# Optimization experiments

Measured on AMD Instinct MI355X. Metric: run time of the kernel, lower is better.

The kernel has to match this reference:

```python
import jax, jax.numpy as jnp
import numpy as np

N_NODES = 100000
H_DIM = 128
N_RELS = 90   # num_rels*2 inside RGCN
N_BASES = 4
N_EDGES = 800000


def setup_inputs() -> dict:
    key = jax.random.key(0)
    k_emb, k_w, k_comp, k_r, k_norm, k_src, k_dst, k_b = jax.random.split(key, 8)
    h = jnp.arange(N_NODES, dtype=jnp.int64 if jax.config.jax_enable_x64 else jnp.int32)
    r = jax.random.randint(k_r, (N_EDGES,), 0, N_RELS)
    norm = jax.random.uniform(k_norm, (N_EDGES, 1), dtype=jnp.float32)
    src = jax.random.randint(k_src, (N_EDGES,), 0, N_NODES)
    dst = jax.random.randint(k_dst, (N_EDGES,), 0, N_NODES)
    # learned params (embedding table stands in for the word2vec-initialized table)
    emb_table = jax.random.normal(k_emb, (N_NODES, H_DIM), dtype=jnp.float32) * 0.02
    weight = jax.random.normal(k_w, (N_BASES, H_DIM, H_DIM), dtype=jnp.float32) * (1.0 / np.sqrt(H_DIM))
    w_comp = jax.random.normal(k_comp, (N_RELS, N_BASES), dtype=jnp.float32) * 0.5
    h_bias = jnp.zeros((H_DIM,), dtype=jnp.float32)
    return {"h": h, "r": r, "norm": norm, "src": src, "dst": dst,
            "emb_table": emb_table, "weight": weight, "w_comp": w_comp, "h_bias": h_bias}


def reference(h, r, norm, src, dst, emb_table, weight, w_comp, h_bias):
    # Input layer: embedding lookup on node ids  -> [N, D]
    x = emb_table[h]
    # Basis decomposition: project node feats onto each basis once  -> [N, B, D]
    # (avoids materializing per-edge [D,D] relation matrices)
    xb = jnp.einsum('ni,bio->nbo', x, weight)
    # Per-edge message: combine basis projections with relation coefficients
    coeff = w_comp[r]                       # [E, B]
    msg = jnp.einsum('ebo,eb->eo', xb[src], coeff)   # [E, D]
    msg = msg * norm                        # edge norm [E,1]
    # scatter-mean over destination nodes
    agg = jax.ops.segment_sum(msg, dst, num_segments=N_NODES)          # [N, D]
    cnt = jax.ops.segment_sum(jnp.ones((msg.shape[0],), msg.dtype), dst,
                              num_segments=N_NODES)                    # [N]
    node_repr = agg / jnp.maximum(cnt, 1.0)[:, None]
    # bias (RelGraphConv default bias=True); activation=None, self_loop=False, dropout=0
    node_repr = node_repr + h_bias
    return node_repr
```

## Files before the change

kernel.cpp:

```cpp
#include <hip/hip_runtime.h>
#include <hip/hip_bf16.h>

#define N_NODES 100000
#define H_DIM   128
#define N_RELS  90
#define N_BASES 4
#define N_EDGES 800000
#define SCAN_NB 391
#define NBLK    6250

typedef __attribute__((ext_vector_type(8))) __bf16 bf16x8;
typedef __attribute__((ext_vector_type(4))) float  floatx4;

#define WT_OFF     0
#define CNTS_OFF   131072
#define OFFS_OFF   531072
#define CURS_OFF   931072
#define BSUM_OFF   1331072
#define BPRE_OFF   1332672
#define RECS_OFF   1334272

__device__ __forceinline__ float bs2f(unsigned short s) {
    union { unsigned u; float f; } x; x.u = ((unsigned)s) << 16; return x.f;
}
__device__ __forceinline__ unsigned short f2bs(float f) {
    unsigned u = __float_as_uint(f);
    return (unsigned short)((u + 0x7fffu + ((u >> 16) & 1u)) >> 16);
}
__device__ __forceinline__ float ldf(const void* p, size_t i, int isbf) {
    return isbf ? bs2f(((const unsigned short*)p)[i]) : ((const float*)p)[i];
}
__device__ __forceinline__ int detect_bf(const void* norm) {
    const unsigned* w = (const unsigned*)norm;
    int hits = 0;
#pragma unroll
    for (int i = 0; i < 16; ++i) {
        unsigned b1 = (w[i] >> 8) & 0xffu;
        hits += (b1 >= 0x30u && b1 <= 0x3fu) ? 1 : 0;
    }
    return hits >= 12;
}

__global__ __launch_bounds__(256) void prep_count_k(const void* __restrict__ weight,
                                                    unsigned short* __restrict__ wt,
                                                    const int* __restrict__ dst,
                                                    int* __restrict__ counts,
                                                    const void* __restrict__ norm) {
    int b = blockIdx.x;
    if (b < 256) {
        int isbf = detect_bf(norm);
        int tid = b * 256 + threadIdx.x;
        int o = tid >> 9, c = tid & 511;
        int bb = c >> 7, i = c & 127;
        wt[tid] = f2bs(ldf(weight, (size_t)bb * 16384 + (size_t)i * 128 + o, isbf));
    } else {
        int e = (b - 256) * 256 + threadIdx.x;
        if (e < N_EDGES) atomicAdd(&counts[dst[e]], 1);
    }
}

__global__ __launch_bounds__(256) void scanA(const int* __restrict__ counts,
                                             int* __restrict__ offs, int* __restrict__ bsum) {
    __shared__ int s[256];
    int t = threadIdx.x, i = blockIdx.x * 256 + t;
    int v = (i < N_NODES) ? counts[i] : 0;
    s[t] = v; __syncthreads();
    for (int off = 1; off < 256; off <<= 1) {
        int x = (t >= off) ? s[t - off] : 0;
        __syncthreads(); s[t] += x; __syncthreads();
    }
    if (i < N_NODES) offs[i] = s[t] - v;
    if (t == 255) bsum[blockIdx.x] = s[255];
}

__global__ __launch_bounds__(512) void scanB(const int* __restrict__ bsum, int* __restrict__ bpre) {
    __shared__ int s[512];
    int t = threadIdx.x;
    int v = (t < SCAN_NB) ? bsum[t] : 0;
    s[t] = v; __syncthreads();
    for (int off = 1; off < 512; off <<= 1) {
        int x = (t >= off) ? s[t - off] : 0;
        __syncthreads(); s[t] += x; __syncthreads();
    }
    if (t < SCAN_NB) bpre[t] = s[t] - v;
}

__global__ __launch_bounds__(256) void scanC(int* __restrict__ offs, const int* __restrict__ bpre,
                                             int* __restrict__ cursor) {
    int i = blockIdx.x * 256 + threadIdx.x;
    if (i < N_NODES) {
        int o = offs[i] + bpre[i >> 8];
        offs[i] = o; cursor[i] = o;
    }
}

__global__ __launch_bounds__(256) void fill_k(const int* __restrict__ r, const void* __restrict__ norm,
                                              const int* __restrict__ src, const int* __restrict__ dst,
                                              const int* __restrict__ h,
                                              int* __restrict__ cursor,
                                              unsigned long long* __restrict__ recs) {
    int e = blockIdx.x * 256 + threadIdx.x;
    if (e >= N_EDGES) return;
    int isbf = detect_bf(norm);
    float nm = ldf(norm, e, isbf);
    unsigned lo = (unsigned)h[src[e]] | ((unsigned)r[e] << 20);
    unsigned long long rc = (unsigned long long)lo
                          | ((unsigned long long)__float_as_uint(nm) << 32);
    int pos = atomicAdd(&cursor[dst[e]], 1);
    __builtin_nontemporal_store(rc, &recs[pos]);
}

__global__ __launch_bounds__(256) void fused_k(const int* __restrict__ counts,
                                               const int* __restrict__ offs,
                                               const unsigned long long* __restrict__ recs,
                                               const void* __restrict__ emb,
                                               const unsigned short* __restrict__ wt,
                                               const void* __restrict__ bias,
                                               const void* __restrict__ wcomp,
                                               const void* __restrict__ norm,
                                               void* __restrict__ out) {
    int isbf = detect_bf(norm);
    __shared__ float wc[N_RELS * 4];
    __shared__ __align__(16) unsigned short y[16][520];
    for (int t = threadIdx.x; t < N_RELS * 4; t += 256) wc[t] = ldf(wcomp, t, isbf);
    __syncthreads();

    int t = threadIdx.x;
    int lane = t & 63;
    int w = t >> 6;
    int g = lane >> 4, j = lane & 15;
    int blk = blockIdx.x;
    int dloc = w * 4 + g;
    int d = blk * 16 + dloc;
    int deg = counts[d], start = offs[d];
    float inv = 1.0f / (float)(deg > 1 ? deg : 1);

    float acc[4][8];
#pragma unroll
    for (int b = 0; b < 4; ++b)
#pragma unroll
        for (int c = 0; c < 8; ++c) acc[b][c] = 0.f;

    int kmax = __shfl(deg, 0);
    kmax = max(kmax, __shfl(deg, 16));
    kmax = max(kmax, __shfl(deg, 32));
    kmax = max(kmax, __shfl(deg, 48));

    unsigned long long rcur[4];
#pragma unroll
    for (int u = 0; u < 4; ++u) rcur[u] = recs[(u < deg) ? start + u : 0];

    for (int k = 0; k < kmax; k += 4) {
        unsigned long long rnext[4];
#pragma unroll
        for (int u = 0; u < 4; ++u) {
            int kk = k + 4 + u;
            rnext[u] = recs[(kk < deg) ? start + kk : 0];
        }
        bf16x8  rb[4];
        floatx4 rf[4][2];
        if (isbf) {
#pragma unroll
            for (int u = 0; u < 4; ++u) {
                unsigned hx = (unsigned)rcur[u] & 0xFFFFFu;
                rb[u] = *(const bf16x8*)((const unsigned short*)emb + (size_t)hx * 128 + j * 8);
            }
        } else {
#pragma unroll
            for (int u = 0; u < 4; ++u) {
                unsigned hx = (unsigned)rcur[u] & 0xFFFFFu;
                const floatx4* f = (const floatx4*)((const float*)emb + (size_t)hx * 128 + j * 8);
                rf[u][0] = f[0]; rf[u][1] = f[1];
            }
        }
#pragma unroll
        for (int u = 0; u < 4; ++u) {
            bool v = (k + u) < deg;
            unsigned rel = ((unsigned)rcur[u] >> 20) & 0xFFFu;
            float nm = v ? __uint_as_float((unsigned)(rcur[u] >> 32)) : 0.f;
            const float* cw = &wc[rel * 4];
            float c0 = cw[0] * nm, c1 = cw[1] * nm, c2 = cw[2] * nm, c3 = cw[3] * nm;
            float x[8];
            if (isbf) {
#pragma unroll
                for (int c = 0; c < 8; ++c) x[c] = (float)rb[u][c];
            } else {
#pragma unroll
                for (int c = 0; c < 4; ++c) { x[c] = rf[u][0][c]; x[c + 4] = rf[u][1][c]; }
            }
#pragma unroll
            for (int c = 0; c < 8; ++c) {
                acc[0][c] += c0 * x[c];
                acc[1][c] += c1 * x[c];
                acc[2][c] += c2 * x[c];
                acc[3][c] += c3 * x[c];
            }
        }
#pragma unroll
        for (int u = 0; u < 4; ++u) rcur[u] = rnext[u];
    }

#pragma unroll
    for (int b = 0; b < 4; ++b) {
        union { unsigned short u[8]; uint4 v; } pk;
#pragma unroll
        for (int c = 0; c < 8; ++c) pk.u[c] = f2bs(acc[b][c] * inv);
        *(uint4*)&y[dloc][b * 128 + j * 8] = pk.v;
    }
    __syncthreads();

    int m = lane & 15;
    int q = lane >> 4;
    for (int half = 0; half < 2; ++half) {
        int ct = w * 2 + half;
        floatx4 accm = {0.f, 0.f, 0.f, 0.f};
        const unsigned short* bp = wt + (size_t)(ct * 16 + m) * 512 + q * 8;
#pragma unroll
        for (int kc = 0; kc < 16; ++kc) {
            bf16x8 af = *(const bf16x8*)&y[m][kc * 32 + q * 8];
            bf16x8 bf = *(const bf16x8*)(bp + kc * 32);
            accm = __builtin_amdgcn_mfma_f32_16x16x32_bf16(af, bf, accm, 0, 0, 0);
        }
#pragma unroll
        for (int v = 0; v < 4; ++v) {
            int o = ct * 16 + m;
            float val = accm[v] + ldf(bias, o, isbf);
            size_t oi = (size_t)(blk * 16 + q * 4 + v) * H_DIM + o;
            if (isbf) ((unsigned short*)out)[oi] = f2bs(val);
            else      ((float*)out)[oi] = val;
        }
    }
}

extern "C" void kernel_launch(void* const* d_in, const int* in_sizes, int n_in,
                              void* d_out, int out_size, void* d_ws, size_t ws_size,
                              hipStream_t stream) {
    const int*  h      = (const int*)d_in[0];
    const int*  r      = (const int*)d_in[1];
    const void* norm   = d_in[2];
    const int*  src    = (const int*)d_in[3];
    const int*  dst    = (const int*)d_in[4];
    const void* emb    = d_in[5];
    const void* weight = d_in[6];
    const void* wcomp  = d_in[7];
    const void* bias   = d_in[8];

    char* ws = (char*)d_ws;
    unsigned short*     wt     = (unsigned short*)(ws + WT_OFF);
    int*                counts = (int*)(ws + CNTS_OFF);
    int*                offs   = (int*)(ws + OFFS_OFF);
    int*                cursor = (int*)(ws + CURS_OFF);
    int*                bsum   = (int*)(ws + BSUM_OFF);
    int*                bpre   = (int*)(ws + BPRE_OFF);
    unsigned long long* recs   = (unsigned long long*)(ws + RECS_OFF);

    hipMemsetAsync(counts, 0, N_NODES * sizeof(int), stream);

    prep_count_k<<<256 + (N_EDGES + 255) / 256, 256, 0, stream>>>(weight, wt, dst, counts, norm);
    scanA<<<SCAN_NB, 256, 0, stream>>>(counts, offs, bsum);
    scanB<<<1, 512, 0, stream>>>(bsum, bpre);
    scanC<<<SCAN_NB, 256, 0, stream>>>(offs, bpre, cursor);
    fill_k<<<(N_EDGES + 255) / 256, 256, 0, stream>>>(r, norm, src, dst, h, cursor, recs);
    fused_k<<<NBLK, 256, 0, stream>>>(counts, offs, recs, emb, wt, bias, wcomp, norm, d_out);
}
```

Baseline: 355.3 us.

## Merge scan stages, template fused kernel on dtype flag, use nontemporal loads/stores

Removes the single-block scanB kernel by having each scanC2 block reduce the preceding block sums itself. The bf16/fp32 detection now runs once in prep_count_k and is stored to a flag, and fused_k is templated on dtype. Both instantiations are launched and the non-matching one exits early. Record loads and output stores become nontemporal. This saves one launch and runtime branching, but adds an extra near-empty 6250-block launch.

```diff
diff --git a/kernel.cpp b/kernel.cpp
--- a/kernel.cpp
+++ b/kernel.cpp
@@ -17,7 +17,7 @@
 #define OFFS_OFF   531072
 #define CURS_OFF   931072
 #define BSUM_OFF   1331072
-#define BPRE_OFF   1332672
+#define FLAG_OFF   1332672
 #define RECS_OFF   1334272
 
 __device__ __forceinline__ float bs2f(unsigned short s) {
@@ -45,8 +45,10 @@
                                                     unsigned short* __restrict__ wt,
                                                     const int* __restrict__ dst,
                                                     int* __restrict__ counts,
-                                                    const void* __restrict__ norm) {
+                                                    const void* __restrict__ norm,
+                                                    int* __restrict__ flag) {
     int b = blockIdx.x;
+    if (b == 0 && threadIdx.x == 0) *flag = detect_bf(norm);
     if (b < 256) {
         int isbf = detect_bf(norm);
         int tid = b * 256 + threadIdx.x;
@@ -73,23 +75,25 @@
     if (t == 255) bsum[blockIdx.x] = s[255];
 }
 
-__global__ __launch_bounds__(512) void scanB(const int* __restrict__ bsum, int* __restrict__ bpre) {
-    __shared__ int s[512];
-    int t = threadIdx.x;
-    int v = (t < SCAN_NB) ? bsum[t] : 0;
-    s[t] = v; __syncthreads();
-    for (int off = 1; off < 512; off <<= 1) {
-        int x = (t >= off) ? s[t - off] : 0;
-        __syncthreads(); s[t] += x; __syncthreads();
-    }
-    if (t < SCAN_NB) bpre[t] = s[t] - v;
-}
-
-__global__ __launch_bounds__(256) void scanC(int* __restrict__ offs, const int* __restrict__ bpre,
-                                             int* __restrict__ cursor) {
-    int i = blockIdx.x * 256 + threadIdx.x;
+__global__ __launch_bounds__(256) void scanC2(int* __restrict__ offs,
+                                              const int* __restrict__ bsum,
+                                              int* __restrict__ cursor) {
+    int b = blockIdx.x, t = threadIdx.x;
+    int v = 0;
+    if (t < b) v = bsum[t];
+    if (t + 256 < b) v += bsum[t + 256];
+    v += __shfl_down(v, 32); v += __shfl_down(v, 16);
+    v += __shfl_down(v, 8);  v += __shfl_down(v, 4);
+    v += __shfl_down(v, 2);  v += __shfl_down(v, 1);
+    __shared__ int wsum[4];
+    __shared__ int sprefix;
+    if ((t & 63) == 0) wsum[t >> 6] = v;
+    __syncthreads();
+    if (t == 0) sprefix = wsum[0] + wsum[1] + wsum[2] + wsum[3];
+    __syncthreads();
+    int i = b * 256 + t;
     if (i < N_NODES) {
-        int o = offs[i] + bpre[i >> 8];
+        int o = offs[i] + sprefix;
         offs[i] = o; cursor[i] = o;
     }
 }
@@ -110,6 +114,7 @@
     __builtin_nontemporal_store(rc, &recs[pos]);
 }
 
+template <int ISBF>
 __global__ __launch_bounds__(256) void fused_k(const int* __restrict__ counts,
                                                const int* __restrict__ offs,
                                                const unsigned long long* __restrict__ recs,
@@ -117,12 +122,12 @@
                                                const unsigned short* __restrict__ wt,
                                                const void* __restrict__ bias,
                                                const void* __restrict__ wcomp,
-                                               const void* __restrict__ norm,
+                                               const int* __restrict__ flag,
                                                void* __restrict__ out) {
-    int isbf = detect_bf(norm);
+    if ((*flag != 0) != (ISBF != 0)) return;
     __shared__ float wc[N_RELS * 4];
     __shared__ __align__(16) unsigned short y[16][520];
-    for (int t = threadIdx.x; t < N_RELS * 4; t += 256) wc[t] = ldf(wcomp, t, isbf);
+    for (int t = threadIdx.x; t < N_RELS * 4; t += 256) wc[t] = ldf(wcomp, t, ISBF);
     __syncthreads();
 
     int t = threadIdx.x;
@@ -148,18 +153,19 @@
 
     unsigned long long rcur[4];
 #pragma unroll
-    for (int u = 0; u < 4; ++u) rcur[u] = recs[(u < deg) ? start + u : 0];
+    for (int u = 0; u < 4; ++u)
+        rcur[u] = __builtin_nontemporal_load(&recs[(u < deg) ? start + u : 0]);
 
     for (int k = 0; k < kmax; k += 4) {
         unsigned long long rnext[4];
 #pragma unroll
         for (int u = 0; u < 4; ++u) {
             int kk = k + 4 + u;
-            rnext[u] = recs[(kk < deg) ? start + kk : 0];
+            rnext[u] = __builtin_nontemporal_load(&recs[(kk < deg) ? start + kk : 0]);
         }
         bf16x8  rb[4];
         floatx4 rf[4][2];
-        if (isbf) {
+        if (ISBF) {
 #pragma unroll
             for (int u = 0; u < 4; ++u) {
                 unsigned hx = (unsigned)rcur[u] & 0xFFFFFu;
@@ -181,7 +187,7 @@
             const float* cw = &wc[rel * 4];
             float c0 = cw[0] * nm, c1 = cw[1] * nm, c2 = cw[2] * nm, c3 = cw[3] * nm;
             float x[8];
-            if (isbf) {
+            if (ISBF) {
 #pragma unroll
                 for (int c = 0; c < 8; ++c) x[c] = (float)rb[u][c];
             } else {
@@ -224,10 +230,10 @@
 #pragma unroll
         for (int v = 0; v < 4; ++v) {
             int o = ct * 16 + m;
-            float val = accm[v] + ldf(bias, o, isbf);
+            float val = accm[v] + ldf(bias, o, ISBF);
             size_t oi = (size_t)(blk * 16 + q * 4 + v) * H_DIM + o;
-            if (isbf) ((unsigned short*)out)[oi] = f2bs(val);
-            else      ((float*)out)[oi] = val;
+            if (ISBF) __builtin_nontemporal_store(f2bs(val), (unsigned short*)out + oi);
+            else      __builtin_nontemporal_store(val, (float*)out + oi);
         }
     }
 }
@@ -251,15 +257,16 @@
     int*                offs   = (int*)(ws + OFFS_OFF);
     int*                cursor = (int*)(ws + CURS_OFF);
     int*                bsum   = (int*)(ws + BSUM_OFF);
-    int*                bpre   = (int*)(ws + BPRE_OFF);
+    int*                flag   = (int*)(ws + FLAG_OFF);
     unsigned long long* recs   = (unsigned long long*)(ws + RECS_OFF);
 
     hipMemsetAsync(counts, 0, N_NODES * sizeof(int), stream);
 
-    prep_count_k<<<256 + (N_EDGES + 255) / 256, 256, 0, stream>>>(weight, wt, dst, counts, norm);
+    prep_count_k<<<256 + (N_EDGES + 255) / 256, 256, 0, stream>>>(weight, wt, dst, counts,
+                                                                  norm, flag);
     scanA<<<SCAN_NB, 256, 0, stream>>>(counts, offs, bsum);
-    scanB<<<1, 512, 0, stream>>>(bsum, bpre);
-    scanC<<<SCAN_NB, 256, 0, stream>>>(offs, bpre, cursor);
+    scanC2<<<SCAN_NB, 256, 0, stream>>>(offs, bsum, cursor);
     fill_k<<<(N_EDGES + 255) / 256, 256, 0, stream>>>(r, norm, src, dst, h, cursor, recs);
-    fused_k<<<NBLK, 256, 0, stream>>>(counts, offs, recs, emb, wt, bias, wcomp, norm, d_out);
-}
+    fused_k<1><<<NBLK, 256, 0, stream>>>(counts, offs, recs, emb, wt, bias, wcomp, flag, d_out);
+    fused_k<0><<<NBLK, 256, 0, stream>>>(counts, offs, recs, emb, wt, bias, wcomp, flag, d_out);
+}
```

Result: faster. 337.7 us (-4.9%).
